# Kernel optimization log

Measured on AMD Instinct MI355X. Metric: run time of the kernel, lower is better.

The kernel has to match this reference:

```python
import jax, jax.numpy as jnp
import numpy as np

# MACE TensorProductConv with in_irreps=128x0e, sh_irreps=0e+1o+2e+3o,
# every CG path 0e (x) l -> l is the identity, so the fused tensor product is
# out[e, c, (l, m)] = w[e, l, c] * x_src[e, c] * sh[e, (l, m)].
# SymmetricContraction is a stub (pass) in the given source, treated as identity.

N_SRC = 10000
N_DST = 10000
E = 100000
C = 128           # channel multiplicity
LS = (0, 1, 2, 3) # spherical-harmonic degrees; dims 1,3,5,7 -> sh dim 16
SH_DIM = sum(2 * l + 1 for l in LS)
MLP_IN = 64
MLP_HID = 128
W_NUMEL = len(LS) * C  # 512 tensor-product weights per edge


def setup_inputs() -> dict:
    key = jax.random.key(0)
    ks = jax.random.split(key, 7)
    return {
        "src_features": jax.random.normal(ks[0], (N_SRC, C), dtype=jnp.float32),
        "edge_sh": jax.random.normal(ks[1], (E, SH_DIM), dtype=jnp.float32),
        "edge_emb": jax.random.normal(ks[2], (E, MLP_IN), dtype=jnp.float32),
        "W1": jax.random.normal(ks[3], (MLP_IN, MLP_HID), dtype=jnp.float32),
        "W2": jax.random.normal(ks[4], (MLP_HID, W_NUMEL), dtype=jnp.float32),
        "src": jax.random.randint(ks[5], (E,), 0, N_SRC),
        "dst": jax.random.randint(ks[6], (E,), 0, N_DST),
        "num_dst_nodes": N_DST,
    }


def _mlp(edge_emb, W1, W2):
    # e3nn FullyConnectedNet: normalized linear layers, silu on hidden only.
    h = jax.nn.silu(edge_emb @ (W1 / np.sqrt(MLP_IN)))
    return h @ (W2 / np.sqrt(MLP_HID))  # [E, W_NUMEL]


def reference(src_features, edge_sh, edge_emb, W1, W2, src, dst, num_dst_nodes):
    tp_w = _mlp(edge_emb, W1, W2).reshape(-1, len(LS), C)  # [E, L, C]
    x_src = src_features[src]                                # gather: [E, C]
    outs = []
    off = 0
    for i, l in enumerate(LS):
        d = 2 * l + 1
        sh_l = edge_sh[:, off:off + d]                       # [E, d]
        # weighted scalar-times-SH tensor product: [E, C, d]
        o = (tp_w[:, i, :] * x_src)[:, :, None] * sh_l[:, None, :]
        outs.append(o.reshape(o.shape[0], C * d))
        off += d
    out_e = jnp.concatenate(outs, axis=-1)                   # [E, 2048]
    # scatter-reduce sum onto destination nodes
    node_out = jax.ops.segment_sum(out_e, dst, num_segments=num_dst_nodes)
    # SymmetricContraction stub -> identity
    return node_out
```

## Files before the change

### kernel.cpp

```cpp
#include <hip/hip_runtime.h>
#include <math.h>

#define C_DIM 128
#define SHD   16
#define HID   128
#define MIN_D 64
#define OUT_PER_NODE 2048
#define BLK   256
#define SCAN_T 1024
#define MT    128

#define EST 72
#define HST 136

typedef __attribute__((ext_vector_type(8))) short bf16x8;
typedef __attribute__((ext_vector_type(4))) float f32x4;

__device__ __forceinline__ unsigned f2bf_u(float x) {
    unsigned u = __builtin_bit_cast(unsigned, x);
    return (u + 0x7fffu + ((u >> 16) & 1u)) >> 16;
}
__device__ __forceinline__ short f2bf(float x) { return (short)f2bf_u(x); }
__device__ __forceinline__ unsigned packbf2(float a, float b) {
    return f2bf_u(a) | (f2bf_u(b) << 16);
}
__device__ __forceinline__ float bf2f(unsigned h) {
    return __builtin_bit_cast(float, h << 16);
}

__global__ void prep_kernel(const int* __restrict__ dst, int* counts, int E,
                            const float* __restrict__ W1, const float* __restrict__ W2,
                            short* __restrict__ w1t, short* __restrict__ w2t,
                            int HB) {
    int b = blockIdx.x;
    int t = threadIdx.x;
    if (b < HB) {
        int i = b * BLK + t;
        if (i < E) atomicAdd(&counts[dst[i]], 1);
    } else {
        int i = (b - HB) * BLK + t;
        if (i < MIN_D * HID) {
            int n = i >> 6, k = i & 63;
            w1t[i] = f2bf(W1[k * HID + n] * 0.125f);
        } else if (i < MIN_D * HID + HID * 512) {
            int j = i - MIN_D * HID;
            int p = j >> 7, ks = j & 127;
            int nt = p >> 4, m16 = p & 15;
            int jcol = 32 * (nt >> 1) + 2 * m16 + (nt & 1);
            int ka   = (2 * (ks >> 5) + (ks & 1)) * 16 + ((ks >> 1) & 15);
            w2t[j] = f2bf(W2[ka * 512 + jcol] * 0.0883883476483184f);
        }
    }
}

__global__ __launch_bounds__(SCAN_T)
void scan_kernel(const int* __restrict__ counts, int* row_ptr, int* cursor, int n) {
    const int t = threadIdx.x;
    const int per = (n + SCAN_T - 1) / SCAN_T;
    int lp[16];
    int base = t * per;
    int sum = 0;
    for (int i = 0; i < per && i < 16; ++i) {
        int idx = base + i;
        int v = (idx < n) ? counts[idx] : 0;
        lp[i] = sum;
        sum += v;
    }
    __shared__ int sbuf[SCAN_T];
    sbuf[t] = sum;
    __syncthreads();
    for (int off = 1; off < SCAN_T; off <<= 1) {
        int v = (t >= off) ? sbuf[t - off] : 0;
        __syncthreads();
        sbuf[t] += v;
        __syncthreads();
    }
    int excl = (t == 0) ? 0 : sbuf[t - 1];
    for (int i = 0; i < per && i < 16; ++i) {
        int idx = base + i;
        if (idx < n) {
            int rp = excl + lp[i];
            row_ptr[idx] = rp;
            cursor[idx]  = rp;
        }
    }
    if (t == SCAN_T - 1) row_ptr[n] = sbuf[SCAN_T - 1];
}

__global__ void scatter_kernel(const int* __restrict__ dst, const int* __restrict__ src,
                               int* cursor, int2* es_list, int E) {
    int i = blockIdx.x * blockDim.x + threadIdx.x;
    if (i < E) {
        int pos = atomicAdd(&cursor[dst[i]], 1);
        es_list[pos] = make_int2(i, src[i]);
    }
}

__global__ __launch_bounds__(BLK)
void mlp_kernel(const float* __restrict__ edge_emb,
                const short* __restrict__ w1t,
                const short* __restrict__ w2t,
                unsigned* __restrict__ tp_u,
                int E)
{
    const int t    = threadIdx.x;
    const int lane = t & 63;
    const int w    = t >> 6;
    const int m16  = lane & 15;
    const int q    = lane >> 4;
    const int e0   = blockIdx.x * MT;

    __shared__ __align__(16) short embb[MT * EST];
    __shared__ __align__(16) short hb  [MT * HST];
    unsigned* embb_u = (unsigned*)embb;
    unsigned* hb_u   = (unsigned*)hb;

    for (int i = t; i < MT * (MIN_D / 4); i += BLK) {
        int row = i >> 4, c4 = (i & 15) << 2;
        float4 v = make_float4(0.f, 0.f, 0.f, 0.f);
        int ge = e0 + row;
        if (ge < E) v = *(const float4*)&edge_emb[(size_t)ge * MIN_D + c4];
        unsigned lo = packbf2(v.x, v.y), hi = packbf2(v.z, v.w);
        embb_u[row * (EST / 2) + (c4 >> 1)]     = lo;
        embb_u[row * (EST / 2) + (c4 >> 1) + 1] = hi;
    }
    __syncthreads();

    {
        bf16x8 a[2][2];
#pragma unroll
        for (int mt2 = 0; mt2 < 2; ++mt2) {
            int mt = w * 2 + mt2;
#pragma unroll
            for (int ks = 0; ks < 2; ++ks)
                a[mt2][ks] = *(const bf16x8*)&embb[(mt * 16 + m16) * EST + ks * 32 + q * 8];
        }
#pragma unroll
        for (int u = 0; u < 4; ++u) {
            bf16x8 b0[2], b1[2];
#pragma unroll
            for (int ks = 0; ks < 2; ++ks) {
                b0[ks] = *(const bf16x8*)&w1t[((2 * u) * 16 + m16) * MIN_D + ks * 32 + q * 8];
                b1[ks] = *(const bf16x8*)&w1t[((2 * u + 1) * 16 + m16) * MIN_D + ks * 32 + q * 8];
            }
#pragma unroll
            for (int mt2 = 0; mt2 < 2; ++mt2) {
                int mt = w * 2 + mt2;
                f32x4 c0 = {0.f, 0.f, 0.f, 0.f}, c1 = {0.f, 0.f, 0.f, 0.f};
#pragma unroll
                for (int ks = 0; ks < 2; ++ks) {
                    c0 = __builtin_amdgcn_mfma_f32_16x16x32_bf16(a[mt2][ks], b0[ks], c0, 0, 0, 0);
                    c1 = __builtin_amdgcn_mfma_f32_16x16x32_bf16(a[mt2][ks], b1[ks], c1, 0, 0, 0);
                }
#pragma unroll
                for (int r = 0; r < 4; ++r) {
                    int row = mt * 16 + q * 4 + r;
                    float z0 = c0[r], z1 = c1[r];
                    float h0 = z0 / (1.f + __expf(-z0));
                    float h1 = z1 / (1.f + __expf(-z1));
                    hb_u[row * (HST / 2) + 16 * u + m16] = packbf2(h0, h1);
                }
            }
        }
    }
    __syncthreads();

    {
        bf16x8 a[2][4];
#pragma unroll
        for (int mt2 = 0; mt2 < 2; ++mt2) {
            int mt = w * 2 + mt2;
#pragma unroll
            for (int ks = 0; ks < 4; ++ks)
                a[mt2][ks] = *(const bf16x8*)&hb[(mt * 16 + m16) * HST + ks * 32 + q * 8];
        }
        for (int u = 0; u < 16; ++u) {
            f32x4 c00 = {0.f,0.f,0.f,0.f}, c01 = {0.f,0.f,0.f,0.f};
            f32x4 c10 = {0.f,0.f,0.f,0.f}, c11 = {0.f,0.f,0.f,0.f};
#pragma unroll
            for (int ks = 0; ks < 4; ++ks) {
                bf16x8 b0 = *(const bf16x8*)&w2t[((2 * u) * 16 + m16) * HID + ks * 32 + q * 8];
                bf16x8 b1 = *(const bf16x8*)&w2t[((2 * u + 1) * 16 + m16) * HID + ks * 32 + q * 8];
                c00 = __builtin_amdgcn_mfma_f32_16x16x32_bf16(a[0][ks], b0, c00, 0, 0, 0);
                c01 = __builtin_amdgcn_mfma_f32_16x16x32_bf16(a[0][ks], b1, c01, 0, 0, 0);
                c10 = __builtin_amdgcn_mfma_f32_16x16x32_bf16(a[1][ks], b0, c10, 0, 0, 0);
                c11 = __builtin_amdgcn_mfma_f32_16x16x32_bf16(a[1][ks], b1, c11, 0, 0, 0);
            }
#pragma unroll
            for (int r = 0; r < 4; ++r) {
                int e = e0 + (w * 2) * 16 + q * 4 + r;
                if (e < E) tp_u[(size_t)e * 256 + 16 * u + m16] = packbf2(c00[r], c01[r]);
                int e2 = e + 16;
                if (e2 < E) tp_u[(size_t)e2 * 256 + 16 * u + m16] = packbf2(c10[r], c11[r]);
            }
        }
    }
}


template<int L>
__device__ __forceinline__ void tp_node(
    const float* __restrict__ src_features,
    const float* __restrict__ edge_sh,
    const unsigned* __restrict__ tp_u,
    const int2* __restrict__ es_list,
    float* __restrict__ out,
    int n, int t, int rbeg, int rend)
{
    constexpr int D = 2 * L + 1;
    constexpr int SHOFF = L * L;
    const int c0 = (2 * t) & 127;
    const int obase = 128 * L * L + c0 * D;

    float accA[D], accB[D];
#pragma unroll
    for (int m = 0; m < D; ++m) { accA[m] = 0.f; accB[m] = 0.f; }

    int i = rbeg;
    for (; i + 4 <= rend; i += 4) {
        int2 es[4];
#pragma unroll
        for (int k = 0; k < 4; ++k) es[k] = es_list[i + k];
        unsigned tp2[4]; float2 x[4]; float sh[4][D];
#pragma unroll
        for (int k = 0; k < 4; ++k) {
            tp2[k] = tp_u[(size_t)es[k].x * 256 + t];
            x[k]   = *(const float2*)&src_features[(size_t)es[k].y * C_DIM + c0];
            const float* shp = &edge_sh[(size_t)es[k].x * SHD + SHOFF];
#pragma unroll
            for (int m = 0; m < D; ++m) sh[k][m] = shp[m];
        }
#pragma unroll
        for (int k = 0; k < 4; ++k) {
            float wx0 = bf2f(tp2[k] & 0xffffu) * x[k].x;
            float wx1 = bf2f(tp2[k] >> 16)     * x[k].y;
#pragma unroll
            for (int m = 0; m < D; ++m) {
                accA[m] += wx0 * sh[k][m];
                accB[m] += wx1 * sh[k][m];
            }
        }
    }
    for (; i < rend; ++i) {
        int2 es = es_list[i];
        unsigned tp2 = tp_u[(size_t)es.x * 256 + t];
        float2 x = *(const float2*)&src_features[(size_t)es.y * C_DIM + c0];
        float wx0 = bf2f(tp2 & 0xffffu) * x.x;
        float wx1 = bf2f(tp2 >> 16)     * x.y;
        const float* shp = &edge_sh[(size_t)es.x * SHD + SHOFF];
#pragma unroll
        for (int m = 0; m < D; ++m) {
            float sh = shp[m];
            accA[m] += wx0 * sh;
            accB[m] += wx1 * sh;
        }
    }

    float* op = out + (size_t)n * OUT_PER_NODE + obase;
#pragma unroll
    for (int m = 0; m < D; ++m) op[m] = accA[m];
#pragma unroll
    for (int m = 0; m < D; ++m) op[D + m] = accB[m];
}

__global__ __launch_bounds__(BLK)
void tp_kernel(const float* __restrict__ src_features,
               const float* __restrict__ edge_sh,
               const unsigned* __restrict__ tp_u,
               const int* __restrict__ row_ptr,
               const int2* __restrict__ es_list,
               float* __restrict__ out)
{
    const int n = blockIdx.x;
    const int t = threadIdx.x;
    const int l = t >> 6;
    const int rbeg = row_ptr[n];
    const int rend = row_ptr[n + 1];
    if (l == 0)      tp_node<0>(src_features, edge_sh, tp_u, es_list, out, n, t, rbeg, rend);
    else if (l == 1) tp_node<1>(src_features, edge_sh, tp_u, es_list, out, n, t, rbeg, rend);
    else if (l == 2) tp_node<2>(src_features, edge_sh, tp_u, es_list, out, n, t, rbeg, rend);
    else             tp_node<3>(src_features, edge_sh, tp_u, es_list, out, n, t, rbeg, rend);
}


extern "C" void kernel_launch(void* const* d_in, const int* in_sizes, int n_in,
                              void* d_out, int out_size, void* d_ws, size_t ws_size,
                              hipStream_t stream) {
    const float* src_features = (const float*)d_in[0];
    const float* edge_sh      = (const float*)d_in[1];
    const float* edge_emb     = (const float*)d_in[2];
    const float* W1           = (const float*)d_in[3];
    const float* W2           = (const float*)d_in[4];
    const int*   src          = (const int*)d_in[5];
    const int*   dst          = (const int*)d_in[6];

    const int E     = in_sizes[5];
    const int N_DST = out_size / OUT_PER_NODE;
    const int EB    = (E + MT - 1) / MT;

    char* p = (char*)d_ws;
    short* w1t      = (short*)p;              p += MIN_D * HID * 2;
    short* w2t      = (short*)p;              p += HID * 512 * 2;
    unsigned* tp_u  = (unsigned*)p;           p += (size_t)EB * MT * 1024;
    int2* es_list   = (int2*)p;               p += (size_t)E * 8;
    int* counts     = (int*)p;                p += 16384 * 4;
    int* row_ptr    = (int*)p;                p += 16384 * 4;
    int* cursor     = (int*)p;                p += 16384 * 4;

    const int HB = (E + BLK - 1) / BLK;
    const int CB = (MIN_D * HID + HID * 512 + BLK - 1) / BLK;

    (void)hipMemsetAsync(counts, 0, (size_t)N_DST * 4, stream);
    prep_kernel<<<HB + CB, BLK, 0, stream>>>(dst, counts, E, W1, W2, w1t, w2t, HB);
    scan_kernel<<<1, SCAN_T, 0, stream>>>(counts, row_ptr, cursor, N_DST);
    scatter_kernel<<<(E + 255) / 256, 256, 0, stream>>>(dst, src, cursor, es_list, E);
    mlp_kernel<<<EB, BLK, 0, stream>>>(edge_emb, w1t, w2t, tp_u, E);
    tp_kernel<<<N_DST, BLK, 0, stream>>>(src_features, edge_sh, tp_u,
                                         row_ptr, es_list, (float*)d_out);
}
```

Baseline: 267.0 us.

## Restructure MLP kernel: 8 waves, register-resident W2 tiles, direct embedding loads

The MLP kernel now runs 512 threads (8 waves) per 128-edge tile. Each wave loads its 16 edge-embedding rows straight from global memory into MFMA operand registers, skipping the shared-memory staging buffer and one barrier. For the second layer, each wave keeps a 64-column slice of W2 in registers and sweeps all 8 row tiles of the hidden activations from LDS, so W2 is no longer re-read per output tile. This trades more registers per thread and more LDS reads of the hidden buffer for fewer global weight loads and more parallelism per block.

```diff
diff --git a/kernel.cpp b/kernel.cpp
--- a/kernel.cpp
+++ b/kernel.cpp
@@ -7,10 +7,10 @@
 #define MIN_D 64
 #define OUT_PER_NODE 2048
 #define BLK   256
+#define MBLK  512
 #define SCAN_T 1024
 #define MT    128
 
-#define EST 72
 #define HST 136
 
 typedef __attribute__((ext_vector_type(8))) short bf16x8;
@@ -96,7 +96,7 @@
     }
 }
 
-__global__ __launch_bounds__(BLK)
+__global__ __launch_bounds__(MBLK)
 void mlp_kernel(const float* __restrict__ edge_emb,
                 const short* __restrict__ w1t,
                 const short* __restrict__ w2t,
@@ -110,93 +110,87 @@
     const int q    = lane >> 4;
     const int e0   = blockIdx.x * MT;
 
-    __shared__ __align__(16) short embb[MT * EST];
-    __shared__ __align__(16) short hb  [MT * HST];
-    unsigned* embb_u = (unsigned*)embb;
-    unsigned* hb_u   = (unsigned*)hb;
-
-    for (int i = t; i < MT * (MIN_D / 4); i += BLK) {
-        int row = i >> 4, c4 = (i & 15) << 2;
-        float4 v = make_float4(0.f, 0.f, 0.f, 0.f);
-        int ge = e0 + row;
-        if (ge < E) v = *(const float4*)&edge_emb[(size_t)ge * MIN_D + c4];
-        unsigned lo = packbf2(v.x, v.y), hi = packbf2(v.z, v.w);
-        embb_u[row * (EST / 2) + (c4 >> 1)]     = lo;
-        embb_u[row * (EST / 2) + (c4 >> 1) + 1] = hi;
-    }
+    __shared__ __align__(16) short hb[MT * HST];
+    unsigned* hb_u = (unsigned*)hb;
+
+    union CVT { unsigned u[4]; bf16x8 v; };
+
+    bf16x8 a[2];
+    {
+        const int row = e0 + w * 16 + m16;
+        if (row < E) {
+            const float* rp = &edge_emb[(size_t)row * MIN_D];
+#pragma unroll
+            for (int ks = 0; ks < 2; ++ks) {
+                float4 v0 = *(const float4*)&rp[ks * 32 + q * 8];
+                float4 v1 = *(const float4*)&rp[ks * 32 + q * 8 + 4];
+                CVT c;
+                c.u[0] = packbf2(v0.x, v0.y);
+                c.u[1] = packbf2(v0.z, v0.w);
+                c.u[2] = packbf2(v1.x, v1.y);
+                c.u[3] = packbf2(v1.z, v1.w);
+                a[ks] = c.v;
+            }
+        } else {
+            CVT c; c.u[0] = c.u[1] = c.u[2] = c.u[3] = 0u;
+            a[0] = c.v; a[1] = c.v;
+        }
+    }
+
+#pragma unroll
+    for (int u2 = 0; u2 < 4; ++u2) {
+        f32x4 c0 = {0.f, 0.f, 0.f, 0.f}, c1 = {0.f, 0.f, 0.f, 0.f};
+#pragma unroll
+        for (int ks = 0; ks < 2; ++ks) {
+            bf16x8 b0 = *(const bf16x8*)&w1t[((2 * u2) * 16 + m16) * MIN_D + ks * 32 + q * 8];
+            bf16x8 b1 = *(const bf16x8*)&w1t[((2 * u2 + 1) * 16 + m16) * MIN_D + ks * 32 + q * 8];
+            c0 = __builtin_amdgcn_mfma_f32_16x16x32_bf16(a[ks], b0, c0, 0, 0, 0);
+            c1 = __builtin_amdgcn_mfma_f32_16x16x32_bf16(a[ks], b1, c1, 0, 0, 0);
+        }
+#pragma unroll
+        for (int r = 0; r < 4; ++r) {
+            int hrow = w * 16 + q * 4 + r;
+            float z0 = c0[r], z1 = c1[r];
+            float h0 = z0 / (1.f + __expf(-z0));
+            float h1 = z1 / (1.f + __expf(-z1));
+            hb_u[hrow * (HST / 2) + 16 * u2 + m16] = packbf2(h0, h1);
+        }
+    }
+
+    bf16x8 B[4][4];
+#pragma unroll
+    for (int j = 0; j < 4; ++j)
+#pragma unroll
+        for (int ks = 0; ks < 4; ++ks)
+            B[j][ks] = *(const bf16x8*)&w2t[((4 * w + j) * 16 + m16) * HID + ks * 32 + q * 8];
+
     __syncthreads();
 
-    {
-        bf16x8 a[2][2];
-#pragma unroll
-        for (int mt2 = 0; mt2 < 2; ++mt2) {
-            int mt = w * 2 + mt2;
-#pragma unroll
-            for (int ks = 0; ks < 2; ++ks)
-                a[mt2][ks] = *(const bf16x8*)&embb[(mt * 16 + m16) * EST + ks * 32 + q * 8];
-        }
-#pragma unroll
-        for (int u = 0; u < 4; ++u) {
-            bf16x8 b0[2], b1[2];
-#pragma unroll
-            for (int ks = 0; ks < 2; ++ks) {
-                b0[ks] = *(const bf16x8*)&w1t[((2 * u) * 16 + m16) * MIN_D + ks * 32 + q * 8];
-                b1[ks] = *(const bf16x8*)&w1t[((2 * u + 1) * 16 + m16) * MIN_D + ks * 32 + q * 8];
+    for (int mt = 0; mt < 8; ++mt) {
+        bf16x8 av[4];
+#pragma unroll
+        for (int ks = 0; ks < 4; ++ks)
+            av[ks] = *(const bf16x8*)&hb[(mt * 16 + m16) * HST + ks * 32 + q * 8];
+        f32x4 acc[4];
+#pragma unroll
+        for (int j = 0; j < 4; ++j) acc[j] = (f32x4){0.f, 0.f, 0.f, 0.f};
+#pragma unroll
+        for (int ks = 0; ks < 4; ++ks)
+#pragma unroll
+            for (int j = 0; j < 4; ++j)
+                acc[j] = __builtin_amdgcn_mfma_f32_16x16x32_bf16(av[ks], B[j][ks], acc[j], 0, 0, 0);
+#pragma unroll
+        for (int i = 0; i < 2; ++i) {
+            const int p = 2 * w + i;
+#pragma unroll
+            for (int r = 0; r < 4; ++r) {
+                int e = e0 + mt * 16 + q * 4 + r;
+                if (e < E)
+                    tp_u[(size_t)e * 256 + 16 * p + m16] = packbf2(acc[2 * i][r], acc[2 * i + 1][r]);
             }
-#pragma unroll
-            for (int mt2 = 0; mt2 < 2; ++mt2) {
-                int mt = w * 2 + mt2;
-                f32x4 c0 = {0.f, 0.f, 0.f, 0.f}, c1 = {0.f, 0.f, 0.f, 0.f};
-#pragma unroll
-                for (int ks = 0; ks < 2; ++ks) {
-                    c0 = __builtin_amdgcn_mfma_f32_16x16x32_bf16(a[mt2][ks], b0[ks], c0, 0, 0, 0);
-                    c1 = __builtin_amdgcn_mfma_f32_16x16x32_bf16(a[mt2][ks], b1[ks], c1, 0, 0, 0);
-                }
-#pragma unroll
-                for (int r = 0; r < 4; ++r) {
-                    int row = mt * 16 + q * 4 + r;
-                    float z0 = c0[r], z1 = c1[r];
-                    float h0 = z0 / (1.f + __expf(-z0));
-                    float h1 = z1 / (1.f + __expf(-z1));
-                    hb_u[row * (HST / 2) + 16 * u + m16] = packbf2(h0, h1);
-                }
-            }
-        }
-    }
-    __syncthreads();
-
-    {
-        bf16x8 a[2][4];
-#pragma unroll
-        for (int mt2 = 0; mt2 < 2; ++mt2) {
-            int mt = w * 2 + mt2;
-#pragma unroll
-            for (int ks = 0; ks < 4; ++ks)
-                a[mt2][ks] = *(const bf16x8*)&hb[(mt * 16 + m16) * HST + ks * 32 + q * 8];
-        }
-        for (int u = 0; u < 16; ++u) {
-            f32x4 c00 = {0.f,0.f,0.f,0.f}, c01 = {0.f,0.f,0.f,0.f};
-            f32x4 c10 = {0.f,0.f,0.f,0.f}, c11 = {0.f,0.f,0.f,0.f};
-#pragma unroll
-            for (int ks = 0; ks < 4; ++ks) {
-                bf16x8 b0 = *(const bf16x8*)&w2t[((2 * u) * 16 + m16) * HID + ks * 32 + q * 8];
-                bf16x8 b1 = *(const bf16x8*)&w2t[((2 * u + 1) * 16 + m16) * HID + ks * 32 + q * 8];
-                c00 = __builtin_amdgcn_mfma_f32_16x16x32_bf16(a[0][ks], b0, c00, 0, 0, 0);
-                c01 = __builtin_amdgcn_mfma_f32_16x16x32_bf16(a[0][ks], b1, c01, 0, 0, 0);
-                c10 = __builtin_amdgcn_mfma_f32_16x16x32_bf16(a[1][ks], b0, c10, 0, 0, 0);
-                c11 = __builtin_amdgcn_mfma_f32_16x16x32_bf16(a[1][ks], b1, c11, 0, 0, 0);
-            }
-#pragma unroll
-            for (int r = 0; r < 4; ++r) {
-                int e = e0 + (w * 2) * 16 + q * 4 + r;
-                if (e < E) tp_u[(size_t)e * 256 + 16 * u + m16] = packbf2(c00[r], c01[r]);
-                int e2 = e + 16;
-                if (e2 < E) tp_u[(size_t)e2 * 256 + 16 * u + m16] = packbf2(c10[r], c11[r]);
-            }
-        }
-    }
-}
-
+        }
+    }
+}
 
 template<int L>
 __device__ __forceinline__ void tp_node(
@@ -314,7 +308,7 @@
     prep_kernel<<<HB + CB, BLK, 0, stream>>>(dst, counts, E, W1, W2, w1t, w2t, HB);
     scan_kernel<<<1, SCAN_T, 0, stream>>>(counts, row_ptr, cursor, N_DST);
     scatter_kernel<<<(E + 255) / 256, 256, 0, stream>>>(dst, src, cursor, es_list, E);
-    mlp_kernel<<<EB, BLK, 0, stream>>>(edge_emb, w1t, w2t, tp_u, E);
+    mlp_kernel<<<EB, MBLK, 0, stream>>>(edge_emb, w1t, w2t, tp_u, E);
     tp_kernel<<<N_DST, BLK, 0, stream>>>(src_features, edge_sh, tp_u,
                                          row_ptr, es_list, (float*)d_out);
 }
```

New measurement: 231.6 us. 1.15x faster.
